# Kernel optimization log

Hardware: AMD Instinct MI355X
Metric: run time of the kernel (lower is better)

## Reference

```python
import jax, jax.numpy as jnp
import numpy as np

B, S, D, M = 2, 4096, 128, 64

def _linear_init(key, shape, fan_in):
    bound = 1.0 / np.sqrt(fan_in)
    return jax.random.uniform(key, shape, jnp.float32, -bound, bound)

def setup_inputs() -> dict:
    key = jax.random.key(0)
    ks = jax.random.split(key, 18)
    x = jax.random.normal(ks[0], (B, S, D), jnp.float32)
    context = jax.random.normal(ks[1], (B, S, D), jnp.float32)
    # per-mechanism params (torch Linear semantics: y = x @ W.T + b)
    Wt = _linear_init(ks[2], (M, D, D), D)   # transform weight, laid out [m, in, out]
    bt = _linear_init(ks[3], (M, D), D)
    char = jax.random.normal(ks[4], (M, D), jnp.float32)  # characteristics [1,1,d] per mech
    Wg = _linear_init(ks[5], (M, D), D)      # timing_gate weight (out=1)
    bg = _linear_init(ks[6], (M,), D)
    Wv = _linear_init(ks[7], (M, D), D)      # victory_detector weight (out=1)
    bv = _linear_init(ks[8], (M,), D)
    O = jax.random.normal(ks[9], (M, M), jnp.float32) * 0.02  # overcoming matrix
    # selector: Linear(2D,2D) -> GELU -> Linear(2D,M)
    W1 = _linear_init(ks[10], (2 * D, 2 * D), 2 * D)
    b1 = _linear_init(ks[11], (2 * D,), 2 * D)
    W2 = _linear_init(ks[12], (2 * D, M), 2 * D)
    b2 = _linear_init(ks[13], (M,), 2 * D)
    # integrate: Linear(2D, D)
    Wi = _linear_init(ks[14], (2 * D, D), 2 * D)
    bi = _linear_init(ks[15], (D,), 2 * D)
    return {"x": x, "context": context, "Wt": Wt, "bt": bt, "char": char,
            "Wg": Wg, "bg": bg, "Wv": Wv, "bv": bv, "O": O,
            "W1": W1, "b1": b1, "W2": W2, "b2": b2, "Wi": Wi, "bi": bi}

def reference(x, context, Wt, bt, char, Wg, bg, Wv, bv, O, W1, b1, W2, b2, Wi, bi):
    # selection scores over mechanisms
    sel_in = jnp.concatenate([x, context], axis=-1)          # [b,s,2d]
    h = jax.nn.gelu(sel_in @ W1 + b1, approximate=False)
    selection_scores = jax.nn.softmax(h @ W2 + b2, axis=-1)  # [b,s,m]
    # all 64 mechanism nodes as one batched GEMM
    transformed = jnp.einsum('bsd,mde->bsme', x, Wt) + bt + char   # [b,s,m,d]
    timing = jax.nn.sigmoid(jnp.einsum('bsd,md->bsm', x, Wg) + bg)  # [b,s,m]
    victory = jax.nn.sigmoid(jnp.einsum('bsme,me->bsm', transformed, Wv) + bv)
    outputs = transformed * timing[..., None]                # [b,s,m,d]
    # strategic overcoming modulation: gate = 1 + tanh(scores @ O)
    gates = 1.0 + jnp.tanh(selection_scores @ O)             # [b,s,m]
    selected = jnp.einsum('bsme,bsm->bse', outputs, gates * selection_scores)
    victory_potential = jnp.sum(victory * selection_scores, axis=-1)  # [b,s]
    integrated = jnp.concatenate([x, selected], axis=-1) @ Wi + bi    # [b,s,d]
    return integrated, victory_potential
```

## Files before the change

### kernel.cpp

```cpp
#include <hip/hip_runtime.h>
#include <hip/hip_bf16.h>


typedef __bf16 bf16_t;
typedef __bf16 bf16x8 __attribute__((ext_vector_type(8)));
typedef float  f32x4  __attribute__((ext_vector_type(4)));

#define WS_WTT      0u
#define WS_W1T      2097152u
#define WS_W2T      2228224u
#define WS_OT       2260992u
#define WS_WG       2269184u
#define WS_U        2285568u
#define WS_CVEC     2301952u
#define WS_BCT      2302208u
#define WS_WIT      2318592u

#define VP_OFF 1048576

__device__ __forceinline__ f32x4 mfma16(bf16x8 a, bf16x8 b, f32x4 c) {
  return __builtin_amdgcn_mfma_f32_16x16x32_bf16(a, b, c, 0, 0, 0);
}

__device__ __forceinline__ float gelu_exact(float v) {
  return 0.5f * v * (1.0f + erff(v * 0.70710678118654752f));
}
__device__ __forceinline__ float sigmoidf_(float v) {
  return 1.0f / (1.0f + __expf(-v));
}

__device__ __forceinline__ bf16x8 cvt8(float4 v0, float4 v1) {
  bf16x8 a;
  a[0] = (bf16_t)v0.x; a[1] = (bf16_t)v0.y; a[2] = (bf16_t)v0.z; a[3] = (bf16_t)v0.w;
  a[4] = (bf16_t)v1.x; a[5] = (bf16_t)v1.y; a[6] = (bf16_t)v1.z; a[7] = (bf16_t)v1.w;
  return a;
}

__global__ __launch_bounds__(256) void kprep(
    const float* __restrict__ Wt, const float* __restrict__ bt,
    const float* __restrict__ ch, const float* __restrict__ Wg,
    const float* __restrict__ Wv, const float* __restrict__ bv,
    const float* __restrict__ O, const float* __restrict__ W1,
    const float* __restrict__ W2, const float* __restrict__ Wi,
    char* __restrict__ ws)
{
  const int bid = blockIdx.x, tid = threadIdx.x;
  if (bid < 128) {
    const int m = bid >> 1, half = bid & 1;
    const float* wtm = Wt + m * 16384;
    bf16_t* wtt = (bf16_t*)(ws + WS_WTT) + m * 16384;
    const int ks = half * 2 + (tid >> 7), e = tid & 127;
    bf16_t tmp[32];
    #pragma unroll
    for (int dd = 0; dd < 32; ++dd)
      tmp[dd] = (bf16_t)wtm[(ks * 32 + dd) * 128 + e];
    bf16_t* dst = wtt + ks * 4096 + e * 32;
    #pragma unroll
    for (int g = 0; g < 4; ++g)
      *(bf16x8*)(dst + g * 8) = *(const bf16x8*)(tmp + g * 8);
  } else if (bid < 144) {
    int base = (bid - 128) * 256 + tid;
    int k = base >> 4, c0 = (base & 15) * 16;
    bf16_t* o = (bf16_t*)(ws + WS_W1T);
    #pragma unroll
    for (int j = 0; j < 16; ++j) o[(c0 + j) * 256 + k] = (bf16_t)W1[k * 256 + c0 + j];
  } else if (bid < 146) {
    int base = (bid - 144) * 256 + tid;
    int k = base >> 1, c0 = (base & 1) * 32;
    bf16_t* o = (bf16_t*)(ws + WS_W2T);
    #pragma unroll
    for (int j = 0; j < 32; ++j) o[(c0 + j) * 256 + k] = (bf16_t)W2[k * 64 + c0 + j];
  } else if (bid == 146) {
    int k = tid >> 2, c0 = (tid & 3) * 16;
    bf16_t* o = (bf16_t*)(ws + WS_OT);
    #pragma unroll
    for (int j = 0; j < 16; ++j) o[(c0 + j) * 64 + k] = (bf16_t)O[k * 64 + c0 + j];
  } else if (bid == 147) {
    bf16_t* o = (bf16_t*)(ws + WS_WG);
    #pragma unroll
    for (int j = 0; j < 32; ++j) o[tid * 32 + j] = (bf16_t)Wg[tid * 32 + j];
  } else if (bid == 148) {
    bf16_t* o = (bf16_t*)(ws + WS_BCT);
    #pragma unroll
    for (int i = 0; i < 4; ++i) {
      int task = tid + i * 256;
      int m = task >> 4, e0 = (task & 15) * 8;
      #pragma unroll
      for (int j = 0; j < 8; ++j)
        o[(e0 + j) * 64 + m] = (bf16_t)(bt[m * 128 + e0 + j] + ch[m * 128 + e0 + j]);
    }
  } else if (bid < 153) {
    int base = (bid - 149) * 256 + tid;
    int k = base >> 2, c0 = (base & 3) * 32;
    bf16_t* o = (bf16_t*)(ws + WS_WIT);
    #pragma unroll
    for (int j = 0; j < 32; ++j) o[(c0 + j) * 256 + k] = (bf16_t)Wi[k * 128 + c0 + j];
  } else if (bid < 185) {
    int task = (bid - 153) * 256 + tid;
    int m = task >> 7, d = task & 127;
    const float4* wp = (const float4*)(Wt + m * 16384 + d * 128);
    const float4* vp = (const float4*)(Wv + m * 128);
    float s = 0.f;
    #pragma unroll
    for (int i = 0; i < 32; ++i) {
      float4 a = wp[i], b = vp[i];
      s += a.x * b.x + a.y * b.y + a.z * b.z + a.w * b.w;
    }
    ((bf16_t*)(ws + WS_U))[m * 128 + d] = (bf16_t)s;
  } else {
    if (tid < 64) {
      int m = tid;
      const float4* bp = (const float4*)(bt + m * 128);
      const float4* cp = (const float4*)(ch + m * 128);
      const float4* vp = (const float4*)(Wv + m * 128);
      float s = bv[m];
      #pragma unroll
      for (int i = 0; i < 32; ++i) {
        float4 a = bp[i], c = cp[i], b = vp[i];
        s += (a.x + c.x) * b.x + (a.y + c.y) * b.y + (a.z + c.z) * b.z + (a.w + c.w) * b.w;
      }
      ((float*)(ws + WS_CVEC))[m] = s;
    }
  }
}

__device__ __forceinline__ void loadF(bf16x8 (&F)[4], const char* bbase, int m) {
  const char* p = bbase + m * 32768;
  F[0] = *(const bf16x8*)(p);
  F[1] = *(const bf16x8*)(p + 8192);
  F[2] = *(const bf16x8*)(p + 16384);
  F[3] = *(const bf16x8*)(p + 24576);
}

#define SM_BYTES 46592

__global__ __launch_bounds__(256, 2) void kfused(
    const float* __restrict__ x, const float* __restrict__ ctx,
    const float* __restrict__ b1, const float* __restrict__ b2,
    const float* __restrict__ bg, const float* __restrict__ bi,
    char* __restrict__ ws, float* __restrict__ out)
{
  __shared__ char sm[SM_BYTES];
  bf16_t* hL      = (bf16_t*)sm;
  float*  scoresL = (float*)(sm + 16384);
  float*  wLT     = (float*)(sm + 24576);
  bf16_t* scbL    = (bf16_t*)(sm + 33792);
  bf16_t* wbL     = (bf16_t*)(sm + 37888);
  bf16_t* selL    = (bf16_t*)(sm + 41984);
  float*  vpL     = (float*)(sm + 46080);

  const int tid = threadIdx.x;
  const int lane = tid & 63, wq = tid >> 6;
  const int tb = (blockIdx.x >> 1) * 32;
  const int eh = blockIdx.x & 1;
  const int lr = lane & 15;
  const int lg = lane >> 4;
  const int lk = lg * 8;
  const int lj4 = lg * 4;

  const bf16_t* W1t = (const bf16_t*)(ws + WS_W1T);
  const bf16_t* W2t = (const bf16_t*)(ws + WS_W2T);
  const bf16_t* Ot  = (const bf16_t*)(ws + WS_OT);
  const bf16_t* Wgb = (const bf16_t*)(ws + WS_WG);
  const bf16_t* Ub  = (const bf16_t*)(ws + WS_U);
  const float*  cv  = (const float*)(ws + WS_CVEC);
  const bf16_t* bct = (const bf16_t*)(ws + WS_BCT);
  const bf16_t* Wit = (const bf16_t*)(ws + WS_WIT);
  const char*  wttc = (const char*)(ws + WS_WTT);

  bf16x8 aX[2][4];
  #pragma unroll
  for (int rg = 0; rg < 2; ++rg) {
    const float* xr = x + (tb + rg * 16 + lr) * 128;
    #pragma unroll
    for (int ks = 0; ks < 4; ++ks)
      aX[rg][ks] = cvt8(*(const float4*)(xr + ks * 32 + lk),
                        *(const float4*)(xr + ks * 32 + lk + 4));
  }

  {
    f32x4 a1[4][2] = {{{0,0,0,0},{0,0,0,0}},{{0,0,0,0},{0,0,0,0}},
                      {{0,0,0,0},{0,0,0,0}},{{0,0,0,0},{0,0,0,0}}};
    #pragma unroll
    for (int ks = 0; ks < 8; ++ks) {
      bf16x8 af[2];
      if (ks < 4) {
        af[0] = aX[0][ks]; af[1] = aX[1][ks];
      } else {
        #pragma unroll
        for (int rg = 0; rg < 2; ++rg) {
          const float* cr = ctx + (tb + rg * 16 + lr) * 128 + (ks - 4) * 32 + lk;
          af[rg] = cvt8(*(const float4*)cr, *(const float4*)(cr + 4));
        }
      }
      #pragma unroll
      for (int cg = 0; cg < 4; ++cg) {
        bf16x8 b = *(const bf16x8*)(W1t + (wq * 64 + cg * 16 + lr) * 256 + ks * 32 + lk);
        a1[cg][0] = mfma16(af[0], b, a1[cg][0]);
        a1[cg][1] = mfma16(af[1], b, a1[cg][1]);
      }
    }
    #pragma unroll
    for (int cg = 0; cg < 4; ++cg) {
      int c = wq * 64 + cg * 16 + lr;
      float bb = b1[c];
      #pragma unroll
      for (int rg = 0; rg < 2; ++rg)
        #pragma unroll
        for (int j = 0; j < 4; ++j) {
          int r = rg * 16 + lj4 + j;
          float v = gelu_exact(a1[cg][rg][j] + bb);
          *(bf16_t*)((char*)hL + ((r * 512 + c * 2) ^ ((r & 7) << 4))) = (bf16_t)v;
        }
    }
  }
  __syncthreads();

  {
    int c = wq * 16 + lr;
    f32x4 l[2] = {{0,0,0,0},{0,0,0,0}};
    #pragma unroll
    for (int ks = 0; ks < 8; ++ks) {
      int k0 = ks * 32 + lk;
      bf16x8 b = *(const bf16x8*)(W2t + c * 256 + k0);
      #pragma unroll
      for (int rg = 0; rg < 2; ++rg) {
        int r = rg * 16 + lr;
        bf16x8 a = *(const bf16x8*)((char*)hL + ((r * 512 + k0 * 2) ^ ((r & 7) << 4)));
        l[rg] = mfma16(a, b, l[rg]);
      }
    }
    float bb = b2[c];
    #pragma unroll
    for (int rg = 0; rg < 2; ++rg)
      #pragma unroll
      for (int j = 0; j < 4; ++j)
        scoresL[(rg * 16 + lj4 + j) * 64 + c] = l[rg][j] + bb;
  }
  __syncthreads();

  {
    int row = tid >> 3, i = tid & 7;
    float v[8];
    #pragma unroll
    for (int j = 0; j < 8; ++j) v[j] = scoresL[row * 64 + i * 8 + j];
    float mx = v[0];
    #pragma unroll
    for (int j = 1; j < 8; ++j) mx = fmaxf(mx, v[j]);
    mx = fmaxf(mx, __shfl_xor(mx, 1));
    mx = fmaxf(mx, __shfl_xor(mx, 2));
    mx = fmaxf(mx, __shfl_xor(mx, 4));
    float sum = 0.f;
    #pragma unroll
    for (int j = 0; j < 8; ++j) { v[j] = __expf(v[j] - mx); sum += v[j]; }
    sum += __shfl_xor(sum, 1);
    sum += __shfl_xor(sum, 2);
    sum += __shfl_xor(sum, 4);
    float inv = 1.0f / sum;
    #pragma unroll
    for (int j = 0; j < 8; ++j) {
      float s = v[j] * inv;
      int cc = i * 8 + j;
      scoresL[row * 64 + cc] = s;
      *(bf16_t*)((char*)scbL + ((row * 128 + cc * 2) ^ ((row & 7) << 4))) = (bf16_t)s;
    }
  }
  __syncthreads();

  {
    const int c = wq * 16 + lr;
    f32x4 g[2] = {{0,0,0,0},{0,0,0,0}};
    #pragma unroll
    for (int ks = 0; ks < 2; ++ks) {
      int k0 = ks * 32 + lk;
      bf16x8 b = *(const bf16x8*)(Ot + c * 64 + k0);
      #pragma unroll
      for (int rg = 0; rg < 2; ++rg) {
        int r = rg * 16 + lr;
        bf16x8 a = *(const bf16x8*)((char*)scbL + ((r * 128 + k0 * 2) ^ ((r & 7) << 4)));
        g[rg] = mfma16(a, b, g[rg]);
      }
    }
    f32x4 t[2] = {{0,0,0,0},{0,0,0,0}};
    f32x4 v[2] = {{0,0,0,0},{0,0,0,0}};
    #pragma unroll
    for (int ks = 0; ks < 4; ++ks) {
      bf16x8 bT = *(const bf16x8*)(Wgb + c * 128 + ks * 32 + lk);
      bf16x8 bV = *(const bf16x8*)(Ub  + c * 128 + ks * 32 + lk);
      #pragma unroll
      for (int rg = 0; rg < 2; ++rg) {
        t[rg] = mfma16(aX[rg][ks], bT, t[rg]);
        v[rg] = mfma16(aX[rg][ks], bV, v[rg]);
      }
    }
    float bgc = bg[c], cvc = cv[c];
    #pragma unroll
    for (int rg = 0; rg < 2; ++rg)
      #pragma unroll
      for (int j = 0; j < 4; ++j) {
        int r = rg * 16 + lj4 + j;
        float gate = 1.0f + tanhf(g[rg][j]);
        float tim  = sigmoidf_(t[rg][j] + bgc);
        float vic  = sigmoidf_(v[rg][j] + cvc);
        float sc   = scoresL[r * 64 + c];
        float w    = gate * sc * tim;
        wLT[c * 36 + r] = w;
        *(bf16_t*)((char*)wbL + ((r * 128 + c * 2) ^ ((r & 7) << 4))) = (bf16_t)w;
        float pv = vic * sc;
        pv += __shfl_xor(pv, 1); pv += __shfl_xor(pv, 2);
        pv += __shfl_xor(pv, 4); pv += __shfl_xor(pv, 8);
        if (lr == 0) vpL[r * 4 + wq] = pv;
      }
  }
  __syncthreads();

  if (eh == 0 && tid < 32) {
    float s = vpL[tid * 4 + 0] + vpL[tid * 4 + 1] + vpL[tid * 4 + 2] + vpL[tid * 4 + 3];
    out[VP_OFF + tb + tid] = s;
  }

  f32x4 acc[2] = {{0,0,0,0},{0,0,0,0}};
  {
    int eg = eh * 64 + wq * 16 + lr;
    #pragma unroll
    for (int ks = 0; ks < 2; ++ks) {
      int k0 = ks * 32 + lk;
      bf16x8 b = *(const bf16x8*)(bct + eg * 64 + k0);
      #pragma unroll
      for (int rg = 0; rg < 2; ++rg) {
        int r = rg * 16 + lr;
        bf16x8 a = *(const bf16x8*)((char*)wbL + ((r * 128 + k0 * 2) ^ ((r & 7) << 4)));
        acc[rg] = mfma16(a, b, acc[rg]);
      }
    }
  }

  const char* bbase = wttc + (size_t)(((eh * 64 + wq * 16 + lr) * 32 + lg * 8) * 2);
  bf16x8 F[8][4];
  loadF(F[0], bbase, 0);
  loadF(F[1], bbase, 1);
  loadF(F[2], bbase, 2);
  loadF(F[3], bbase, 3);
  loadF(F[4], bbase, 4);
  loadF(F[5], bbase, 5);

  #pragma unroll
  for (int it = 0; it < 8; ++it) {
    const int base = it * 8;
    #pragma unroll
    for (int s = 0; s < 8; ++s) {
      const int m = base + s;
      int mp = m + 6; if (mp > 63) mp = 63;
      loadF(F[(s + 6) & 7], bbase, mp);
      f32x4 w0 = *(const f32x4*)(&wLT[m * 36 + lj4]);
      f32x4 w1 = *(const f32x4*)(&wLT[m * 36 + 16 + lj4]);
      f32x4 y0 = {0.f,0.f,0.f,0.f}, y1 = {0.f,0.f,0.f,0.f};
      #pragma unroll
      for (int ks = 0; ks < 4; ++ks) {
        y0 = mfma16(aX[0][ks], F[s][ks], y0);
        y1 = mfma16(aX[1][ks], F[s][ks], y1);
      }
      #pragma unroll
      for (int jj = 0; jj < 4; ++jj) {
        acc[0][jj] += w0[jj] * y0[jj];
        acc[1][jj] += w1[jj] * y1[jj];
      }
    }
  }

  #pragma unroll
  for (int rg = 0; rg < 2; ++rg)
    #pragma unroll
    for (int j = 0; j < 4; ++j) {
      int r = rg * 16 + lj4 + j;
      int cl = wq * 16 + lr;
      *(bf16_t*)((char*)selL + ((r * 128 + cl * 2) ^ ((r & 7) << 4))) = (bf16_t)acc[rg][j];
    }
  __syncthreads();

  #pragma unroll
  for (int cg = 0; cg < 2; ++cg) {
    int c = wq * 32 + cg * 16 + lr;
    f32x4 a[2] = {{0,0,0,0},{0,0,0,0}};
    #pragma unroll
    for (int ks = 0; ks < 2; ++ks) {
      int k0 = ks * 32 + lk;
      bf16x8 b = *(const bf16x8*)(Wit + c * 256 + 128 + eh * 64 + k0);
      #pragma unroll
      for (int rg = 0; rg < 2; ++rg) {
        int r = rg * 16 + lr;
        bf16x8 av = *(const bf16x8*)((char*)selL + ((r * 128 + k0 * 2) ^ ((r & 7) << 4)));
        a[rg] = mfma16(av, b, a[rg]);
      }
    }
    if (eh == 0) {
      #pragma unroll
      for (int ks = 0; ks < 4; ++ks) {
        bf16x8 b = *(const bf16x8*)(Wit + c * 256 + ks * 32 + lk);
        #pragma unroll
        for (int rg = 0; rg < 2; ++rg) a[rg] = mfma16(aX[rg][ks], b, a[rg]);
      }
    }
    float bb = (eh == 0) ? bi[c] : 0.0f;
    #pragma unroll
    for (int rg = 0; rg < 2; ++rg)
      #pragma unroll
      for (int j = 0; j < 4; ++j)
        atomicAdd(&out[(tb + rg * 16 + lj4 + j) * 128 + c], a[rg][j] + bb);
  }
}

extern "C" void kernel_launch(void* const* d_in, const int* in_sizes, int n_in,
                              void* d_out, int out_size, void* d_ws, size_t ws_size,
                              hipStream_t stream)
{
  (void)in_sizes; (void)n_in; (void)ws_size;
  const float* x   = (const float*)d_in[0];
  const float* ctx = (const float*)d_in[1];
  const float* Wt  = (const float*)d_in[2];
  const float* bt  = (const float*)d_in[3];
  const float* ch  = (const float*)d_in[4];
  const float* Wg  = (const float*)d_in[5];
  const float* bg  = (const float*)d_in[6];
  const float* Wv  = (const float*)d_in[7];
  const float* bv  = (const float*)d_in[8];
  const float* O   = (const float*)d_in[9];
  const float* W1  = (const float*)d_in[10];
  const float* b1  = (const float*)d_in[11];
  const float* W2  = (const float*)d_in[12];
  const float* b2  = (const float*)d_in[13];
  const float* Wi  = (const float*)d_in[14];
  const float* bi  = (const float*)d_in[15];
  float* out = (float*)d_out;
  char* ws = (char*)d_ws;

  hipMemsetAsync(d_out, 0, (size_t)out_size * 4, stream);
  kprep<<<186, 256, 0, stream>>>(Wt, bt, ch, Wg, Wv, bv, O, W1, W2, Wi, ws);
  kfused<<<512, 256, 0, stream>>>(x, ctx, b1, b2, bg, bi, ws, out);
}
```

Baseline: 156.3 us.

## Split fused kernel into select, mechanism and integrate stages with larger token tiles

Splits the single fused kernel into three kernels. The first computes selection scores and weights once per 32-token tile instead of twice. The second runs the mechanism GEMM on 64-token tiles split across mechanism halves and output halves, so each streamed Wt fragment is reused by more tokens. The third sums partial selections through global workspace and applies the integration GEMM with plain stores, which removes the memset and the atomics. It also replaces erf and tanh with polynomial and exp approximations; the cost is extra launches and workspace round trips.

```diff
diff --git a/kernel.cpp b/kernel.cpp
--- a/kernel.cpp
+++ b/kernel.cpp
@@ -15,6 +15,10 @@
 #define WS_CVEC     2301952u
 #define WS_BCT      2302208u
 #define WS_WIT      2318592u
+#define WS_WT       2384128u
+#define WS_SBIAS    4481280u
+#define WS_SEL0     8675584u
+#define WS_SEL1     12869888u
 
 #define VP_OFF 1048576
 
@@ -22,8 +26,21 @@
   return __builtin_amdgcn_mfma_f32_16x16x32_bf16(a, b, c, 0, 0, 0);
 }
 
-__device__ __forceinline__ float gelu_exact(float v) {
-  return 0.5f * v * (1.0f + erff(v * 0.70710678118654752f));
+__device__ __forceinline__ float erf_fast(float x) {
+  float ax = fabsf(x);
+  float t = 1.0f / (1.0f + 0.3275911f * ax);
+  float p = t * (0.254829592f + t * (-0.284496736f + t * (1.421413741f +
+            t * (-1.453152027f + t * 1.061405429f))));
+  float y = 1.0f - p * __expf(-ax * ax);
+  return copysignf(y, x);
+}
+__device__ __forceinline__ float gelu_fast(float v) {
+  return 0.5f * v * (1.0f + erf_fast(v * 0.70710678118654752f));
+}
+__device__ __forceinline__ float tanh_fast(float x) {
+  float xc = fminf(fmaxf(x, -15.f), 15.f);
+  float e = __expf(2.0f * xc);
+  return (e - 1.0f) / (e + 1.0f);
 }
 __device__ __forceinline__ float sigmoidf_(float v) {
   return 1.0f / (1.0f + __expf(-v));
@@ -124,39 +141,25 @@
   }
 }
 
-__device__ __forceinline__ void loadF(bf16x8 (&F)[4], const char* bbase, int m) {
-  const char* p = bbase + m * 32768;
-  F[0] = *(const bf16x8*)(p);
-  F[1] = *(const bf16x8*)(p + 8192);
-  F[2] = *(const bf16x8*)(p + 16384);
-  F[3] = *(const bf16x8*)(p + 24576);
-}
-
-#define SM_BYTES 46592
-
-__global__ __launch_bounds__(256, 2) void kfused(
+__global__ __launch_bounds__(256) void kselect(
     const float* __restrict__ x, const float* __restrict__ ctx,
     const float* __restrict__ b1, const float* __restrict__ b2,
-    const float* __restrict__ bg, const float* __restrict__ bi,
+    const float* __restrict__ bg,
     char* __restrict__ ws, float* __restrict__ out)
 {
-  __shared__ char sm[SM_BYTES];
+  __shared__ char sm[43008];
   bf16_t* hL      = (bf16_t*)sm;
   float*  scoresL = (float*)(sm + 16384);
   float*  wLT     = (float*)(sm + 24576);
   bf16_t* scbL    = (bf16_t*)(sm + 33792);
   bf16_t* wbL     = (bf16_t*)(sm + 37888);
-  bf16_t* selL    = (bf16_t*)(sm + 41984);
-  float*  vpL     = (float*)(sm + 46080);
+  float*  vpL     = (float*)(sm + 41984);
 
   const int tid = threadIdx.x;
   const int lane = tid & 63, wq = tid >> 6;
-  const int tb = (blockIdx.x >> 1) * 32;
-  const int eh = blockIdx.x & 1;
-  const int lr = lane & 15;
-  const int lg = lane >> 4;
-  const int lk = lg * 8;
-  const int lj4 = lg * 4;
+  const int tb = blockIdx.x * 32;
+  const int lr = lane & 15, lg = lane >> 4;
+  const int lk = lg * 8, lj4 = lg * 4;
 
   const bf16_t* W1t = (const bf16_t*)(ws + WS_W1T);
   const bf16_t* W2t = (const bf16_t*)(ws + WS_W2T);
@@ -165,8 +168,8 @@
   const bf16_t* Ub  = (const bf16_t*)(ws + WS_U);
   const float*  cv  = (const float*)(ws + WS_CVEC);
   const bf16_t* bct = (const bf16_t*)(ws + WS_BCT);
-  const bf16_t* Wit = (const bf16_t*)(ws + WS_WIT);
-  const char*  wttc = (const char*)(ws + WS_WTT);
+  float* wT    = (float*)(ws + WS_WT);
+  float* sbOut = (float*)(ws + WS_SBIAS);
 
   bf16x8 aX[2][4];
   #pragma unroll
@@ -209,7 +212,7 @@
         #pragma unroll
         for (int j = 0; j < 4; ++j) {
           int r = rg * 16 + lj4 + j;
-          float v = gelu_exact(a1[cg][rg][j] + bb);
+          float v = gelu_fast(a1[cg][rg][j] + bb);
           *(bf16_t*)((char*)hL + ((r * 512 + c * 2) ^ ((r & 7) << 4))) = (bf16_t)v;
         }
     }
@@ -299,7 +302,7 @@
       #pragma unroll
       for (int j = 0; j < 4; ++j) {
         int r = rg * 16 + lj4 + j;
-        float gate = 1.0f + tanhf(g[rg][j]);
+        float gate = 1.0f + tanh_fast(g[rg][j]);
         float tim  = sigmoidf_(t[rg][j] + bgc);
         float vic  = sigmoidf_(v[rg][j] + cvc);
         float sc   = scoresL[r * 64 + c];
@@ -314,14 +317,21 @@
   }
   __syncthreads();
 
-  if (eh == 0 && tid < 32) {
+  if (tid < 32) {
     float s = vpL[tid * 4 + 0] + vpL[tid * 4 + 1] + vpL[tid * 4 + 2] + vpL[tid * 4 + 3];
     out[VP_OFF + tb + tid] = s;
   }
-
-  f32x4 acc[2] = {{0,0,0,0},{0,0,0,0}};
   {
-    int eg = eh * 64 + wq * 16 + lr;
+    int m = tid >> 2, r0 = (tid & 3) * 8;
+    float4 v0 = *(const float4*)&wLT[m * 36 + r0];
+    float4 v1 = *(const float4*)&wLT[m * 36 + r0 + 4];
+    *(float4*)&wT[m * 8192 + tb + r0] = v0;
+    *(float4*)&wT[m * 8192 + tb + r0 + 4] = v1;
+  }
+  #pragma unroll
+  for (int cg = 0; cg < 2; ++cg) {
+    int eg = wq * 32 + cg * 16 + lr;
+    f32x4 s[2] = {{0,0,0,0},{0,0,0,0}};
     #pragma unroll
     for (int ks = 0; ks < 2; ++ks) {
       int k0 = ks * 32 + lk;
@@ -330,83 +340,165 @@
       for (int rg = 0; rg < 2; ++rg) {
         int r = rg * 16 + lr;
         bf16x8 a = *(const bf16x8*)((char*)wbL + ((r * 128 + k0 * 2) ^ ((r & 7) << 4)));
-        acc[rg] = mfma16(a, b, acc[rg]);
-      }
-    }
-  }
-
-  const char* bbase = wttc + (size_t)(((eh * 64 + wq * 16 + lr) * 32 + lg * 8) * 2);
-  bf16x8 F[8][4];
-  loadF(F[0], bbase, 0);
-  loadF(F[1], bbase, 1);
-  loadF(F[2], bbase, 2);
-  loadF(F[3], bbase, 3);
-  loadF(F[4], bbase, 4);
-  loadF(F[5], bbase, 5);
+        s[rg] = mfma16(a, b, s[rg]);
+      }
+    }
+    #pragma unroll
+    for (int rg = 0; rg < 2; ++rg)
+      #pragma unroll
+      for (int j = 0; j < 4; ++j)
+        sbOut[(tb + rg * 16 + lj4 + j) * 128 + eg] = s[rg][j];
+  }
+}
+
+__device__ __forceinline__ void loadF(bf16x8 (&F)[4], const char* bbase, int mm) {
+  const char* p = bbase + mm * 32768;
+  F[0] = *(const bf16x8*)(p);
+  F[1] = *(const bf16x8*)(p + 8192);
+  F[2] = *(const bf16x8*)(p + 16384);
+  F[3] = *(const bf16x8*)(p + 24576);
+}
+
+__device__ __forceinline__ void stepM(const bf16x8 (&F)[4], const float* wrow,
+                                      const bf16x8 (&aX)[4][4], f32x4 (&acc)[4], int lj4) {
+  f32x4 y[4] = {{0,0,0,0},{0,0,0,0},{0,0,0,0},{0,0,0,0}};
+  #pragma unroll
+  for (int ks = 0; ks < 4; ++ks) {
+    y[0] = mfma16(aX[0][ks], F[ks], y[0]);
+    y[1] = mfma16(aX[1][ks], F[ks], y[1]);
+    y[2] = mfma16(aX[2][ks], F[ks], y[2]);
+    y[3] = mfma16(aX[3][ks], F[ks], y[3]);
+  }
+  #pragma unroll
+  for (int rg = 0; rg < 4; ++rg) {
+    f32x4 wv = *(const f32x4*)(wrow + rg * 16 + lj4);
+    #pragma unroll
+    for (int jj = 0; jj < 4; ++jj)
+      acc[rg][jj] += wv[jj] * y[rg][jj];
+  }
+}
+
+__global__ __launch_bounds__(256, 2) void kmech(
+    const float* __restrict__ x, char* __restrict__ ws)
+{
+  __shared__ float wmT[32 * 68];
+  const int tid = threadIdx.x;
+  const int lane = tid & 63, wq = tid >> 6;
+  const int b = blockIdx.x;
+  const int tile = b >> 2, eh = (b >> 1) & 1, mh = b & 1;
+  const int tb = tile * 64;
+  const int lr = lane & 15, lg = lane >> 4;
+  const int lk = lg * 8, lj4 = lg * 4;
+
+  const char* wttc = (const char*)(ws + WS_WTT);
+  const float* wT = (const float*)(ws + WS_WT);
+  float* selOut = (float*)(ws + (mh ? WS_SEL1 : WS_SEL0));
+
+  {
+    int mm = tid >> 3, r0 = (tid & 7) * 8;
+    const float* src = wT + (mh * 32 + mm) * 8192 + tb + r0;
+    float4 a = *(const float4*)src, c = *(const float4*)(src + 4);
+    *(float4*)&wmT[mm * 68 + r0] = a;
+    *(float4*)&wmT[mm * 68 + r0 + 4] = c;
+  }
+  bf16x8 aX[4][4];
+  #pragma unroll
+  for (int rg = 0; rg < 4; ++rg) {
+    const float* xr = x + (tb + rg * 16 + lr) * 128;
+    #pragma unroll
+    for (int ks = 0; ks < 4; ++ks)
+      aX[rg][ks] = cvt8(*(const float4*)(xr + ks * 32 + lk),
+                        *(const float4*)(xr + ks * 32 + lk + 4));
+  }
+  f32x4 acc[4] = {{0,0,0,0},{0,0,0,0},{0,0,0,0},{0,0,0,0}};
+  __syncthreads();
+
+  const char* bbase = wttc + (size_t)(mh * 32) * 32768
+                    + (size_t)(((eh * 64 + wq * 16 + lr) * 32 + lg * 8) * 2);
+  bf16x8 F0[4], F1[4], F2[4], F3[4];
+  loadF(F0, bbase, 0);
+  loadF(F1, bbase, 1);
+  loadF(F2, bbase, 2);
 
   #pragma unroll
   for (int it = 0; it < 8; ++it) {
-    const int base = it * 8;
-    #pragma unroll
-    for (int s = 0; s < 8; ++s) {
-      const int m = base + s;
-      int mp = m + 6; if (mp > 63) mp = 63;
-      loadF(F[(s + 6) & 7], bbase, mp);
-      f32x4 w0 = *(const f32x4*)(&wLT[m * 36 + lj4]);
-      f32x4 w1 = *(const f32x4*)(&wLT[m * 36 + 16 + lj4]);
-      f32x4 y0 = {0.f,0.f,0.f,0.f}, y1 = {0.f,0.f,0.f,0.f};
-      #pragma unroll
-      for (int ks = 0; ks < 4; ++ks) {
-        y0 = mfma16(aX[0][ks], F[s][ks], y0);
-        y1 = mfma16(aX[1][ks], F[s][ks], y1);
-      }
-      #pragma unroll
-      for (int jj = 0; jj < 4; ++jj) {
-        acc[0][jj] += w0[jj] * y0[jj];
-        acc[1][jj] += w1[jj] * y1[jj];
-      }
-    }
-  }
-
-  #pragma unroll
-  for (int rg = 0; rg < 2; ++rg)
-    #pragma unroll
-    for (int j = 0; j < 4; ++j) {
-      int r = rg * 16 + lj4 + j;
-      int cl = wq * 16 + lr;
-      *(bf16_t*)((char*)selL + ((r * 128 + cl * 2) ^ ((r & 7) << 4))) = (bf16_t)acc[rg][j];
-    }
-  __syncthreads();
-
+    const int base = it * 4;
+    const int n3 = base + 3;
+    const int n4 = base + 4 > 31 ? 31 : base + 4;
+    const int n5 = base + 5 > 31 ? 31 : base + 5;
+    const int n6 = base + 6 > 31 ? 31 : base + 6;
+    loadF(F3, bbase, n3);
+    stepM(F0, &wmT[(base + 0) * 68], aX, acc, lj4);
+    loadF(F0, bbase, n4);
+    stepM(F1, &wmT[(base + 1) * 68], aX, acc, lj4);
+    loadF(F1, bbase, n5);
+    stepM(F2, &wmT[(base + 2) * 68], aX, acc, lj4);
+    loadF(F2, bbase, n6);
+    stepM(F3, &wmT[(base + 3) * 68], aX, acc, lj4);
+  }
+
+  #pragma unroll
+  for (int rg = 0; rg < 4; ++rg)
+    #pragma unroll
+    for (int j = 0; j < 4; ++j)
+      selOut[(tb + rg * 16 + lj4 + j) * 128 + eh * 64 + wq * 16 + lr] = acc[rg][j];
+}
+
+__global__ __launch_bounds__(256) void kinteg(
+    const float* __restrict__ x, const float* __restrict__ bi,
+    const char* __restrict__ ws, float* __restrict__ out)
+{
+  const int tid = threadIdx.x;
+  const int lane = tid & 63, wq = tid >> 6;
+  const int tb = blockIdx.x * 32;
+  const int lr = lane & 15, lg = lane >> 4;
+  const int lk = lg * 8, lj4 = lg * 4;
+  const bf16_t* Wit = (const bf16_t*)(ws + WS_WIT);
+  const float* s0 = (const float*)(ws + WS_SEL0);
+  const float* s1 = (const float*)(ws + WS_SEL1);
+  const float* sb = (const float*)(ws + WS_SBIAS);
+
+  bf16x8 aF[2][8];
+  #pragma unroll
+  for (int rg = 0; rg < 2; ++rg) {
+    int t = tb + rg * 16 + lr;
+    #pragma unroll
+    for (int ks = 0; ks < 4; ++ks) {
+      const float* src = x + t * 128 + ks * 32 + lk;
+      aF[rg][ks] = cvt8(*(const float4*)src, *(const float4*)(src + 4));
+    }
+    #pragma unroll
+    for (int ks = 0; ks < 4; ++ks) {
+      int idx = t * 128 + ks * 32 + lk;
+      float4 a0 = *(const float4*)(s0 + idx);
+      float4 a1 = *(const float4*)(s1 + idx);
+      float4 a2 = *(const float4*)(sb + idx);
+      float4 b0 = *(const float4*)(s0 + idx + 4);
+      float4 b1 = *(const float4*)(s1 + idx + 4);
+      float4 b2 = *(const float4*)(sb + idx + 4);
+      float4 u; u.x = a0.x + a1.x + a2.x; u.y = a0.y + a1.y + a2.y;
+      u.z = a0.z + a1.z + a2.z; u.w = a0.w + a1.w + a2.w;
+      float4 v; v.x = b0.x + b1.x + b2.x; v.y = b0.y + b1.y + b2.y;
+      v.z = b0.z + b1.z + b2.z; v.w = b0.w + b1.w + b2.w;
+      aF[rg][4 + ks] = cvt8(u, v);
+    }
+  }
   #pragma unroll
   for (int cg = 0; cg < 2; ++cg) {
     int c = wq * 32 + cg * 16 + lr;
-    f32x4 a[2] = {{0,0,0,0},{0,0,0,0}};
-    #pragma unroll
-    for (int ks = 0; ks < 2; ++ks) {
-      int k0 = ks * 32 + lk;
-      bf16x8 b = *(const bf16x8*)(Wit + c * 256 + 128 + eh * 64 + k0);
-      #pragma unroll
-      for (int rg = 0; rg < 2; ++rg) {
-        int r = rg * 16 + lr;
-        bf16x8 av = *(const bf16x8*)((char*)selL + ((r * 128 + k0 * 2) ^ ((r & 7) << 4)));
-        a[rg] = mfma16(av, b, a[rg]);
-      }
-    }
-    if (eh == 0) {
-      #pragma unroll
-      for (int ks = 0; ks < 4; ++ks) {
-        bf16x8 b = *(const bf16x8*)(Wit + c * 256 + ks * 32 + lk);
-        #pragma unroll
-        for (int rg = 0; rg < 2; ++rg) a[rg] = mfma16(aX[rg][ks], b, a[rg]);
-      }
-    }
-    float bb = (eh == 0) ? bi[c] : 0.0f;
-    #pragma unroll
-    for (int rg = 0; rg < 2; ++rg)
-      #pragma unroll
-      for (int j = 0; j < 4; ++j)
-        atomicAdd(&out[(tb + rg * 16 + lj4 + j) * 128 + c], a[rg][j] + bb);
+    f32x4 a0 = {0,0,0,0}, a1 = {0,0,0,0};
+    #pragma unroll
+    for (int ks = 0; ks < 8; ++ks) {
+      bf16x8 b = *(const bf16x8*)(Wit + c * 256 + ks * 32 + lk);
+      a0 = mfma16(aF[0][ks], b, a0);
+      a1 = mfma16(aF[1][ks], b, a1);
+    }
+    float bb = bi[c];
+    #pragma unroll
+    for (int j = 0; j < 4; ++j) {
+      out[(tb + lj4 + j) * 128 + c] = a0[j] + bb;
+      out[(tb + 16 + lj4 + j) * 128 + c] = a1[j] + bb;
+    }
   }
 }
 
@@ -414,7 +506,7 @@
                               void* d_out, int out_size, void* d_ws, size_t ws_size,
                               hipStream_t stream)
 {
-  (void)in_sizes; (void)n_in; (void)ws_size;
+  (void)in_sizes; (void)n_in; (void)out_size; (void)ws_size;
   const float* x   = (const float*)d_in[0];
   const float* ctx = (const float*)d_in[1];
   const float* Wt  = (const float*)d_in[2];
@@ -434,7 +526,8 @@
   float* out = (float*)d_out;
   char* ws = (char*)d_ws;
 
-  hipMemsetAsync(d_out, 0, (size_t)out_size * 4, stream);
   kprep<<<186, 256, 0, stream>>>(Wt, bt, ch, Wg, Wv, bv, O, W1, W2, Wi, ws);
-  kfused<<<512, 256, 0, stream>>>(x, ctx, b1, b2, bg, bi, ws, out);
-}
+  kselect<<<256, 256, 0, stream>>>(x, ctx, b1, b2, bg, ws, out);
+  kmech<<<512, 256, 0, stream>>>(x, ws);
+  kinteg<<<256, 256, 0, stream>>>(x, bi, ws, out);
+}
```

Measured after the change: 152.7 us. 2.3% less time.
